# Optimization experiments

Hardware: AMD Instinct MI355X
Metric: run time of the kernel (lower is better)

## Reference

```python
import jax, jax.numpy as jnp
import numpy as np

B, T, D, H = 4, 2048, 512, 8
K = D // H  # head dim = 64

def setup_inputs() -> dict:
    key = jax.random.key(0)
    k1, k2, k3, k4 = jax.random.split(key, 4)
    x = jax.random.normal(k1, (B, T, D), dtype=jnp.float32)
    # torch nn.Linear stores weight as [out_features, in_features]
    w_qkv = jax.random.normal(k2, (3 * D, D), dtype=jnp.float32) * (D ** -0.5)
    w_proj = jax.random.normal(k3, (D, D), dtype=jnp.float32) * (D ** -0.5)
    b_proj = jax.random.normal(k4, (D,), dtype=jnp.float32) * 0.01
    return {"x": x, "w_qkv": w_qkv, "w_proj": w_proj, "b_proj": b_proj}

def reference(x, w_qkv, w_proj, b_proj):
    Bx, Tx, Dx = x.shape
    # qkv projection (no bias): [B,T,3D]
    qkv = jnp.einsum('btd,ed->bte', x, w_qkv)
    q, k, v = jnp.split(qkv, 3, axis=-1)
    # [B,H,T,K]
    def heads(t):
        return t.reshape(Bx, Tx, H, K).transpose(0, 2, 1, 3)
    q, k, v = heads(q), heads(k), heads(v)
    # scaled scores with causal mask
    scores = jnp.einsum('bhqk,bhsk->bhqs', q, k) * (K ** -0.5)  # [B,H,T,T]
    causal = jnp.tril(jnp.ones((Tx, Tx), dtype=bool))
    scores = jnp.where(causal, scores, -jnp.inf)
    attn = jax.nn.softmax(scores, axis=-1)  # dropout p=0.0 -> identity
    out = jnp.einsum('bhqs,bhsk->bhqk', attn, v)  # [B,H,T,K]
    out = out.transpose(0, 2, 1, 3).reshape(Bx, Tx, Dx)
    out = jnp.einsum('btd,ed->bte', out, w_proj) + b_proj
    return out
```

## Files before the change

kernel.cpp:

```cpp
#include <hip/hip_runtime.h>
#include <hip/hip_bf16.h>


typedef unsigned short u16;
typedef __attribute__((ext_vector_type(8))) __bf16 bf16x8;
typedef __attribute__((ext_vector_type(8))) unsigned short u16x8;
typedef __attribute__((ext_vector_type(4))) unsigned short u16x4;
typedef __attribute__((ext_vector_type(4))) float f32x4;
typedef __attribute__((ext_vector_type(4))) unsigned u32x4;
typedef __attribute__((ext_vector_type(2))) unsigned u32x2;

#define DEV static __device__ __forceinline__

DEV void async16(const u16* g, u16* l) {
  __builtin_amdgcn_global_load_lds(
      (const __attribute__((address_space(1))) unsigned int*)g,
      (__attribute__((address_space(3))) unsigned int*)l, 16, 0, 0);
}
DEV u16x8 gld8(const u16* p) { return *(const u16x8*)p; }
DEV void lst8(u16* p, u16x8 v) { *(u16x8*)p = v; }
DEV bf16x8 ldsld8(const u16* p) {
  return __builtin_bit_cast(bf16x8, *(const u16x8*)p);
}
DEV f32x4 mfma16(bf16x8 a, bf16x8 b, f32x4 c) {
  return __builtin_amdgcn_mfma_f32_16x16x32_bf16(a, b, c, 0, 0, 0);
}
DEV u16 f2b(float f) {
  unsigned u = __builtin_bit_cast(unsigned, f);
  u += 0x7FFFu + ((u >> 16) & 1u);
  return (u16)(u >> 16);
}
DEV unsigned pk2(float x, float y) {
  __hip_bfloat162 t = __float22bfloat162_rn(float2{x, y});
  unsigned r;
  __builtin_memcpy(&r, &t, 4);
  return r;
}
DEV u16x8 pack8(f32x4 a, f32x4 b) {
  u32x4 t;
  t[0] = pk2(a[0], a[1]);
  t[1] = pk2(a[2], a[3]);
  t[2] = pk2(b[0], b[1]);
  t[3] = pk2(b[2], b[3]);
  return __builtin_bit_cast(u16x8, t);
}
DEV void barrier_lgkm() {
  asm volatile("s_waitcnt lgkmcnt(0)" ::: "memory");
  __builtin_amdgcn_s_barrier();
  asm volatile("" ::: "memory");
}

__global__ void cvt_all(const float* __restrict__ x, const float* __restrict__ wq,
                        u16* __restrict__ xb, u16* __restrict__ wqb) {
  constexpr long NX = 8192L * 512 / 8;
  constexpr long NQ = 1536L * 512 / 8;
  const long i = (long)blockIdx.x * 256 + threadIdx.x;
  if (i < NX) {
    const float* p = x + i * 8;
    *(u16x8*)(xb + i * 8) = pack8(*(const f32x4*)p, *(const f32x4*)(p + 4));
  } else if (i < NX + NQ) {
    const long j = i - NX;
    const float* p = wq + j * 8;
    *(u16x8*)(wqb + j * 8) = pack8(*(const f32x4*)p, *(const f32x4*)(p + 4));
  }
}

__global__ void gemm_bb(const u16* __restrict__ A, const u16* __restrict__ Bt,
                        u16* __restrict__ qk, u16* __restrict__ vT, int K) {
  __shared__ __align__(16) u16 smem[17408];
  auto As = (u16(*)[128 * 32])smem;
  auto Bs = (u16(*)[128 * 32])(smem + 8192);
  u16* Cs = smem;
  constexpr int LDC = 136;

  const int t = threadIdx.x, lane = t & 63, w = t >> 6;
  const int lane15 = lane & 15, quad = lane >> 4;
  const int wr = w >> 1, wc = w & 1;

  const int i = blockIdx.x;
  const int rt = (i & 7) | (((i >> 3) & 7) << 3);
  const int ct = i >> 6;
  const long row0 = (long)rt * 128;
  const int col0 = ct * 128;

  const int srow = w * 16 + (lane >> 2);
  const int scol = (lane & 3) * 8;
  const u16* Ag = A + (row0 + srow) * (long)K + scol;
  const u16* Bg = Bt + ((long)col0 + srow) * (long)K + scol;

  f32x4 acc[4][4];
#pragma unroll
  for (int ii = 0; ii < 4; ii++)
#pragma unroll
    for (int j = 0; j < 4; j++) acc[ii][j] = (f32x4)(0.0f);

  for (int k0 = 0; k0 < K; k0 += 64) {
    __syncthreads();
#pragma unroll
    for (int r = 0; r < 2; r++)
#pragma unroll
      for (int hf = 0; hf < 2; hf++) {
        async16(Ag + (long)r * 64 * K + k0 + hf * 32,
                &As[hf][(r * 64 + w * 16) * 32]);
        async16(Bg + (long)r * 64 * K + k0 + hf * 32,
                &Bs[hf][(r * 64 + w * 16) * 32]);
      }
    __syncthreads();

#pragma unroll
    for (int hf = 0; hf < 2; hf++) {
      bf16x8 a[4], b[4];
#pragma unroll
      for (int ii = 0; ii < 4; ii++)
        a[ii] = ldsld8(&As[hf][(wr * 64 + ii * 16 + lane15) * 32 + quad * 8]);
#pragma unroll
      for (int j = 0; j < 4; j++)
        b[j] = ldsld8(&Bs[hf][(wc * 64 + j * 16 + lane15) * 32 + quad * 8]);
#pragma unroll
      for (int ii = 0; ii < 4; ii++)
#pragma unroll
        for (int j = 0; j < 4; j++) acc[ii][j] = mfma16(a[ii], b[j], acc[ii][j]);
    }
  }

  __syncthreads();

  if (col0 >= 1024) {
#pragma unroll
    for (int ii = 0; ii < 4; ii++)
#pragma unroll
      for (int j = 0; j < 4; j++) {
        const int d = wc * 64 + j * 16 + lane15;
        const int sl = wr * 64 + ii * 16 + quad * 4;
        const int psl =
            (sl & ~31) | (((sl >> 2) & 3) << 3) | (((sl >> 4) & 1) << 2);
        u32x2 pr;
        pr[0] = pk2(acc[ii][j][0], acc[ii][j][1]);
        pr[1] = pk2(acc[ii][j][2], acc[ii][j][3]);
        *(u16x4*)&Cs[d * LDC + psl] = __builtin_bit_cast(u16x4, pr);
      }
    __syncthreads();
    const long bb = row0 >> 11;
    const int s0g = (int)(row0 & 2047);
    const int rr = t >> 4, cc = (t & 15) * 8;
#pragma unroll
    for (int p = 0; p < 8; p++) {
      const int d = p * 16 + rr;
      *(u16x8*)(vT + ((bb * 512 + col0 - 1024 + d) * 2048L) + s0g + cc) =
          *(const u16x8*)&Cs[d * LDC + cc];
    }
  } else {
#pragma unroll
    for (int ii = 0; ii < 4; ii++)
#pragma unroll
      for (int j = 0; j < 4; j++) {
        const int c = wc * 64 + j * 16 + lane15;
        const float sc = (col0 + c < 512) ? 0.18033688f : 1.0f;
#pragma unroll
        for (int r = 0; r < 4; r++) {
          const int rw = wr * 64 + ii * 16 + quad * 4 + r;
          Cs[rw * LDC + c] = f2b(acc[ii][j][r] * sc);
        }
      }
    __syncthreads();
    const int rr = t >> 4, cc = (t & 15) * 8;
#pragma unroll
    for (int p = 0; p < 8; p++) {
      const int rw = p * 16 + rr;
      *(u16x8*)(qk + (row0 + rw) * 1024L + col0 + cc) =
          *(const u16x8*)&Cs[rw * LDC + cc];
    }
  }
}

__global__ void gemm_b64(const u16* __restrict__ A, const float* __restrict__ Bt,
                         const float* __restrict__ bias, float* __restrict__ C,
                         int N, int K) {
  __shared__ __align__(16) u16 smem[17408];
  auto As = (u16(*)[128 * 32])smem;
  auto Bs = (u16(*)[64 * 32])(smem + 8192);
  float* Cs = (float*)smem;
  constexpr int LDCF = 68;

  const int t = threadIdx.x, lane = t & 63, w = t >> 6;
  const int lane15 = lane & 15, quad = lane >> 4;
  const int wr = w >> 1, wc = w & 1;

  const int i = blockIdx.x;
  const int rt = (i & 7) | (((i >> 3) & 7) << 3);
  const int ct = i >> 6;
  const long row0 = (long)rt * 128;
  const int col0 = ct * 64;

  const int srow = w * 16 + (lane >> 2);
  const int scol = (lane & 3) * 8;
  const u16* Ag = A + (row0 + srow) * (long)K + scol;

  const int brow = t >> 2, bc = (t & 3) * 16;
  const float* Bg = Bt + (long)(col0 + brow) * K + bc;
  u16* BsD = &Bs[bc >> 5][brow * 32 + (bc & 31)];

  f32x4 acc[4][2];
#pragma unroll
  for (int ii = 0; ii < 4; ii++)
#pragma unroll
    for (int j = 0; j < 2; j++) acc[ii][j] = (f32x4)(0.0f);

  f32x4 q0 = *(const f32x4*)Bg, q1 = *(const f32x4*)(Bg + 4);
  f32x4 q2 = *(const f32x4*)(Bg + 8), q3 = *(const f32x4*)(Bg + 12);

  for (int k0 = 0; k0 < K; k0 += 64) {
    barrier_lgkm();
#pragma unroll
    for (int r = 0; r < 2; r++)
#pragma unroll
      for (int hf = 0; hf < 2; hf++)
        async16(Ag + (long)r * 64 * K + k0 + hf * 32,
                &As[hf][(r * 64 + w * 16) * 32]);
    lst8(BsD, pack8(q0, q1));
    lst8(BsD + 8, pack8(q2, q3));
    __syncthreads();

    {
      const int kp = (k0 + 64 < K) ? k0 + 64 : k0;
      q0 = *(const f32x4*)(Bg + kp);     q1 = *(const f32x4*)(Bg + kp + 4);
      q2 = *(const f32x4*)(Bg + kp + 8); q3 = *(const f32x4*)(Bg + kp + 12);
    }

#pragma unroll
    for (int hf = 0; hf < 2; hf++) {
      bf16x8 a[4], b[2];
#pragma unroll
      for (int ii = 0; ii < 4; ii++)
        a[ii] = ldsld8(&As[hf][(wr * 64 + ii * 16 + lane15) * 32 + quad * 8]);
#pragma unroll
      for (int j = 0; j < 2; j++)
        b[j] = ldsld8(&Bs[hf][(wc * 32 + j * 16 + lane15) * 32 + quad * 8]);
#pragma unroll
      for (int ii = 0; ii < 4; ii++)
#pragma unroll
        for (int j = 0; j < 2; j++) acc[ii][j] = mfma16(a[ii], b[j], acc[ii][j]);
    }
  }

  __syncthreads();
#pragma unroll
  for (int ii = 0; ii < 4; ii++)
#pragma unroll
    for (int j = 0; j < 2; j++) {
      const int c = wc * 32 + j * 16 + lane15;
      const float bv = bias[col0 + c];
#pragma unroll
      for (int r = 0; r < 4; r++) {
        const int rw = wr * 64 + ii * 16 + quad * 4 + r;
        Cs[rw * LDCF + c] = acc[ii][j][r] + bv;
      }
    }
  __syncthreads();
  const int rr = t >> 4, cc = (t & 15) * 4;
#pragma unroll
  for (int p = 0; p < 8; p++) {
    const int rw = p * 16 + rr;
    *(f32x4*)(C + (row0 + rw) * (long)N + col0 + cc) =
        *(const f32x4*)&Cs[rw * LDCF + cc];
  }
}

__global__ void __launch_bounds__(512, 4)
attn_v10(const u16* __restrict__ qk, const u16* __restrict__ vT,
         u16* __restrict__ out) {
  constexpr int T = 2048, LDQ = 1024;
  __shared__ __align__(16) u16 Ks[2][2][64 * 72];
  __shared__ __align__(16) u16 Vs[2][2][64 * 72];

  const int t = threadIdx.x, lane = t & 63, w = t >> 6;
  const int lane15 = lane & 15, quad = lane >> 4;
  const int half = w >> 2, wl = w & 3;

  const int i = blockIdx.x;
  int qb = i & 15;
  if (i >= 256) qb = 15 - qb;
  const int h = (i >> 4) & 7;
  const int b = (i >> 7) & 3;
  const long baseq = (long)b * T * LDQ;
  const u16* vTb = vT + ((long)b * 512 + h * 64) * 2048;

  const u16* gq =
      qk + baseq + (long)(qb * 128 + wl * 32 + lane15) * LDQ + h * 64 + quad * 8;
  const bf16x8 qa0 = __builtin_bit_cast(bf16x8, *(const u16x8*)gq);
  const bf16x8 qa1 = __builtin_bit_cast(bf16x8, *(const u16x8*)(gq + 32));
  const bf16x8 qc0 = __builtin_bit_cast(bf16x8, *(const u16x8*)(gq + 16 * LDQ));
  const bf16x8 qc1 =
      __builtin_bit_cast(bf16x8, *(const u16x8*)(gq + 16 * LDQ + 32));

  const int th = t & 255;
  const int srow = th >> 3, sc8 = (th & 7) * 8;
  const int nsbh = qb + 1;
  const int s0 = half * nsbh;
  const int sbd = 2 * qb + (wl >> 1);

  const u16* gk = qk + baseq + (long)(s0 * 64 + srow) * LDQ + 512 + h * 64 + sc8;
  const u16* gv = vTb + (long)srow * 2048 + s0 * 64 + sc8;

  u16x8 kr0, kr1, vr0, vr1;
  kr0 = gld8(gk); kr1 = gld8(gk + (long)32 * LDQ);
  vr0 = gld8(gv); vr1 = gld8(gv + (long)32 * 2048);
  lst8(&Ks[half][0][srow * 72 + sc8], kr0);
  lst8(&Ks[half][0][(srow + 32) * 72 + sc8], kr1);
  lst8(&Vs[half][0][srow * 72 + sc8], vr0);
  lst8(&Vs[half][0][(srow + 32) * 72 + sc8], vr1);
  if (nsbh > 1) { gk += (long)64 * LDQ; gv += 64; }
  kr0 = gld8(gk); kr1 = gld8(gk + (long)32 * LDQ);
  vr0 = gld8(gv); vr1 = gld8(gv + (long)32 * 2048);

  f32x4 o0[4], o1[4], lsum0 = (f32x4)(0.0f), lsum1 = (f32x4)(0.0f);
#pragma unroll
  for (int j = 0; j < 4; j++) { o0[j] = (f32x4)(0.0f); o1[j] = (f32x4)(0.0f); }

  const bf16x8 ones = __builtin_bit_cast(bf16x8, (u16x8)((u16)0x3F80));
  const int ql0 = ((wl & 1) << 5) + lane15;

  for (int it = 0; it < nsbh; ++it) {
    const u16* Kc = Ks[half][it & 1];
    const u16* Vc = Vs[half][it & 1];
    u16* Kn = Ks[half][(it + 1) & 1];
    u16* Vn = Vs[half][(it + 1) & 1];

    barrier_lgkm();

    lst8(&Kn[srow * 72 + sc8], kr0);
    lst8(&Kn[(srow + 32) * 72 + sc8], kr1);
    lst8(&Vn[srow * 72 + sc8], vr0);
    lst8(&Vn[(srow + 32) * 72 + sc8], vr1);

    if (it + 2 < nsbh) { gk += (long)64 * LDQ; gv += 64; }
    kr0 = gld8(gk); kr1 = gld8(gk + (long)32 * LDQ);
    vr0 = gld8(gv); vr1 = gld8(gv + (long)32 * 2048);

    const int sb = s0 + it;
    if (sb <= sbd) {
      __builtin_amdgcn_s_setprio(1);
      f32x4 sf0[4], sf1[4];
#pragma unroll
      for (int j = 0; j < 4; j++) {
        const bf16x8 k0 = ldsld8(&Kc[(j * 16 + lane15) * 72 + quad * 8]);
        const bf16x8 k1 = ldsld8(&Kc[(j * 16 + lane15) * 72 + quad * 8 + 32]);
        sf0[j] = mfma16(k1, qa1, mfma16(k0, qa0, (f32x4)(0.0f)));
        sf1[j] = mfma16(k1, qc1, mfma16(k0, qc0, (f32x4)(0.0f)));
      }

#pragma unroll
      for (int j = 0; j < 4; j++)
#pragma unroll
        for (int r = 0; r < 4; r++) {
          sf0[j][r] = exp2f(sf0[j][r]);
          sf1[j][r] = exp2f(sf1[j][r]);
        }
      if (sb == sbd) {
#pragma unroll
        for (int j = 0; j < 4; j++)
#pragma unroll
          for (int r = 0; r < 4; r++) {
            const int sl = j * 16 + quad * 4 + r;
            if (sl > ql0) sf0[j][r] = 0.0f;
            if (sl > ql0 + 16) sf1[j][r] = 0.0f;
          }
      }

      u32x4 w0, w1, w2, w3;
      w0[0] = pk2(sf0[0][0], sf0[0][1]); w0[1] = pk2(sf0[0][2], sf0[0][3]);
      w0[2] = pk2(sf0[1][0], sf0[1][1]); w0[3] = pk2(sf0[1][2], sf0[1][3]);
      w1[0] = pk2(sf0[2][0], sf0[2][1]); w1[1] = pk2(sf0[2][2], sf0[2][3]);
      w1[2] = pk2(sf0[3][0], sf0[3][1]); w1[3] = pk2(sf0[3][2], sf0[3][3]);
      w2[0] = pk2(sf1[0][0], sf1[0][1]); w2[1] = pk2(sf1[0][2], sf1[0][3]);
      w2[2] = pk2(sf1[1][0], sf1[1][1]); w2[3] = pk2(sf1[1][2], sf1[1][3]);
      w3[0] = pk2(sf1[2][0], sf1[2][1]); w3[1] = pk2(sf1[2][2], sf1[2][3]);
      w3[2] = pk2(sf1[3][0], sf1[3][1]); w3[3] = pk2(sf1[3][2], sf1[3][3]);
      const bf16x8 pa0 = __builtin_bit_cast(bf16x8, w0);
      const bf16x8 pa1 = __builtin_bit_cast(bf16x8, w1);
      const bf16x8 pc0 = __builtin_bit_cast(bf16x8, w2);
      const bf16x8 pc1 = __builtin_bit_cast(bf16x8, w3);

#pragma unroll
      for (int j = 0; j < 4; j++) {
        const int d0 = (j * 16 + lane15) * 72;
        const bf16x8 v0 = ldsld8(&Vc[d0 + quad * 8]);
        const bf16x8 v1 = ldsld8(&Vc[d0 + quad * 8 + 32]);
        o0[j] = mfma16(pa1, v1, mfma16(pa0, v0, o0[j]));
        o1[j] = mfma16(pc1, v1, mfma16(pc0, v0, o1[j]));
      }
      lsum0 = mfma16(pa1, ones, mfma16(pa0, ones, lsum0));
      lsum1 = mfma16(pc1, ones, mfma16(pc0, ones, lsum1));
      __builtin_amdgcn_s_setprio(0);
    }
  }

  barrier_lgkm();
  float* cmb = (float*)&Ks[0][0][0];
  float* cl = (float*)&Vs[0][0][0];

  if (half == 1) {
    const int q0 = wl * 32 + quad * 4;
#pragma unroll
    for (int j = 0; j < 4; j++)
#pragma unroll
      for (int r = 0; r < 4; r++) {
        cmb[(q0 + r) * 64 + j * 16 + lane15] = o0[j][r];
        cmb[(q0 + 16 + r) * 64 + j * 16 + lane15] = o1[j][r];
      }
    if (lane15 == 0) {
#pragma unroll
      for (int r = 0; r < 4; r++) {
        cl[q0 + r] = lsum0[r];
        cl[q0 + 16 + r] = lsum1[r];
      }
    }
  }
  barrier_lgkm();

  if (half == 0) {
    const int q0 = wl * 32 + quad * 4;
    f32x4 inv0, inv1;
#pragma unroll
    for (int r = 0; r < 4; r++) {
      inv0[r] = 1.0f / (lsum0[r] + cl[q0 + r]);
      inv1[r] = 1.0f / (lsum1[r] + cl[q0 + 16 + r]);
    }
    const long orow0 = (long)b * T + qb * 128 + wl * 32;
#pragma unroll
    for (int j = 0; j < 4; j++)
#pragma unroll
      for (int r = 0; r < 4; r++) {
        const float a0 = o0[j][r] + cmb[(q0 + r) * 64 + j * 16 + lane15];
        const float a1 = o1[j][r] + cmb[(q0 + 16 + r) * 64 + j * 16 + lane15];
        const long rr = orow0 + quad * 4 + r;
        out[rr * 512 + h * 64 + j * 16 + lane15] = f2b(a0 * inv0[r]);
        out[(rr + 16) * 512 + h * 64 + j * 16 + lane15] = f2b(a1 * inv1[r]);
      }
  }
}

extern "C" void kernel_launch(void* const* d_in, const int* in_sizes, int n_in,
                              void* d_out, int out_size, void* d_ws, size_t ws_size,
                              hipStream_t stream) {
  const float* x      = (const float*)d_in[0];
  const float* w_qkv  = (const float*)d_in[1];
  const float* w_proj = (const float*)d_in[2];
  const float* b_proj = (const float*)d_in[3];
  float* out = (float*)d_out;

  u16* qk = (u16*)d_ws;
  u16* vT = qk + (size_t)8192 * 1024;
  u16* xb = vT + (size_t)4 * 512 * 2048;
  u16* wqb = (u16*)d_out;

  cvt_all<<<2432, 256, 0, stream>>>(x, w_qkv, xb, wqb);
  gemm_bb<<<768, 256, 0, stream>>>(xb, wqb, qk, vT, 512);
  attn_v10<<<512, 512, 0, stream>>>(qk, vT, xb);
  gemm_b64<<<512, 256, 0, stream>>>(xb, w_proj, b_proj, out, 512, 512);
}
```

Before: 142.8 us.

## Load K/V tiles with async global-to-LDS copies and an XOR-swizzled layout

The attention kernel now copies K and V tiles straight from global memory into LDS with global_load_lds, replacing the old path that loaded into registers and then stored to LDS. The padded 72-element row stride is replaced by an unpadded 64-element stride with an XOR swizzle of 16-byte chunks, and the reads are remapped to match. The goal is to drop the register staging and the separate LDS store instructions while avoiding bank conflicts with a smaller LDS footprint. In exchange, the prefetch now only overlaps with one iteration of compute, because the next __syncthreads waits for the async loads. The smaller K/V buffers are also reused as scratch for the final combine, which could be too small.

```diff
diff --git a/kernel.cpp b/kernel.cpp
--- a/kernel.cpp
+++ b/kernel.cpp
@@ -267,11 +267,11 @@
 }
 
 __global__ void __launch_bounds__(512, 4)
-attn_v10(const u16* __restrict__ qk, const u16* __restrict__ vT,
+attn_v11(const u16* __restrict__ qk, const u16* __restrict__ vT,
          u16* __restrict__ out) {
   constexpr int T = 2048, LDQ = 1024;
-  __shared__ __align__(16) u16 Ks[2][2][64 * 72];
-  __shared__ __align__(16) u16 Vs[2][2][64 * 72];
+  __shared__ __align__(16) u16 Ks[2][2][64 * 64];
+  __shared__ __align__(16) u16 Vs[2][2][64 * 64];
 
   const int t = threadIdx.x, lane = t & 63, w = t >> 6;
   const int lane15 = lane & 15, quad = lane >> 4;
@@ -294,24 +294,24 @@
       __builtin_bit_cast(bf16x8, *(const u16x8*)(gq + 16 * LDQ + 32));
 
   const int th = t & 255;
-  const int srow = th >> 3, sc8 = (th & 7) * 8;
+  const int srow = th >> 3;
+  const int scs = (th & 7) ^ (srow & 7);
   const int nsbh = qb + 1;
   const int s0 = half * nsbh;
   const int sbd = 2 * qb + (wl >> 1);
 
-  const u16* gk = qk + baseq + (long)(s0 * 64 + srow) * LDQ + 512 + h * 64 + sc8;
-  const u16* gv = vTb + (long)srow * 2048 + s0 * 64 + sc8;
-
-  u16x8 kr0, kr1, vr0, vr1;
-  kr0 = gld8(gk); kr1 = gld8(gk + (long)32 * LDQ);
-  vr0 = gld8(gv); vr1 = gld8(gv + (long)32 * 2048);
-  lst8(&Ks[half][0][srow * 72 + sc8], kr0);
-  lst8(&Ks[half][0][(srow + 32) * 72 + sc8], kr1);
-  lst8(&Vs[half][0][srow * 72 + sc8], vr0);
-  lst8(&Vs[half][0][(srow + 32) * 72 + sc8], vr1);
-  if (nsbh > 1) { gk += (long)64 * LDQ; gv += 64; }
-  kr0 = gld8(gk); kr1 = gld8(gk + (long)32 * LDQ);
-  vr0 = gld8(gv); vr1 = gld8(gv + (long)32 * 2048);
+  const u16* ksrc = qk + baseq + (long)(s0 * 64 + srow) * LDQ + 512 + h * 64 + scs * 8;
+  const u16* vsrc = vTb + (long)srow * 2048 + s0 * 64 + scs * 8;
+  const int ldst = th * 8;
+
+  {
+    u16* kd = &Ks[half][0][0];
+    u16* vd = &Vs[half][0][0];
+    async16(ksrc, kd + ldst);
+    async16(ksrc + (long)32 * LDQ, kd + 2048 + ldst);
+    async16(vsrc, vd + ldst);
+    async16(vsrc + (long)32 * 2048, vd + 2048 + ldst);
+  }
 
   f32x4 o0[4], o1[4], lsum0 = (f32x4)(0.0f), lsum1 = (f32x4)(0.0f);
 #pragma unroll
@@ -319,32 +319,33 @@
 
   const bf16x8 ones = __builtin_bit_cast(bf16x8, (u16x8)((u16)0x3F80));
   const int ql0 = ((wl & 1) << 5) + lane15;
+  const int cs = (quad ^ (lane15 & 7)) * 8;
 
   for (int it = 0; it < nsbh; ++it) {
-    const u16* Kc = Ks[half][it & 1];
-    const u16* Vc = Vs[half][it & 1];
-    u16* Kn = Ks[half][(it + 1) & 1];
-    u16* Vn = Vs[half][(it + 1) & 1];
-
-    barrier_lgkm();
-
-    lst8(&Kn[srow * 72 + sc8], kr0);
-    lst8(&Kn[(srow + 32) * 72 + sc8], kr1);
-    lst8(&Vn[srow * 72 + sc8], vr0);
-    lst8(&Vn[(srow + 32) * 72 + sc8], vr1);
-
-    if (it + 2 < nsbh) { gk += (long)64 * LDQ; gv += 64; }
-    kr0 = gld8(gk); kr1 = gld8(gk + (long)32 * LDQ);
-    vr0 = gld8(gv); vr1 = gld8(gv + (long)32 * 2048);
+    __syncthreads();
+
+    if (it + 1 < nsbh) {
+      ksrc += (long)64 * LDQ;
+      vsrc += 64;
+      u16* kd = &Ks[half][(it + 1) & 1][0];
+      u16* vd = &Vs[half][(it + 1) & 1][0];
+      async16(ksrc, kd + ldst);
+      async16(ksrc + (long)32 * LDQ, kd + 2048 + ldst);
+      async16(vsrc, vd + ldst);
+      async16(vsrc + (long)32 * 2048, vd + 2048 + ldst);
+    }
 
     const int sb = s0 + it;
     if (sb <= sbd) {
+      const u16* Kc = Ks[half][it & 1];
+      const u16* Vc = Vs[half][it & 1];
       __builtin_amdgcn_s_setprio(1);
       f32x4 sf0[4], sf1[4];
 #pragma unroll
       for (int j = 0; j < 4; j++) {
-        const bf16x8 k0 = ldsld8(&Kc[(j * 16 + lane15) * 72 + quad * 8]);
-        const bf16x8 k1 = ldsld8(&Kc[(j * 16 + lane15) * 72 + quad * 8 + 32]);
+        const int rb = (j * 16 + lane15) * 64;
+        const bf16x8 k0 = ldsld8(&Kc[rb + cs]);
+        const bf16x8 k1 = ldsld8(&Kc[rb + (cs ^ 32)]);
         sf0[j] = mfma16(k1, qa1, mfma16(k0, qa0, (f32x4)(0.0f)));
         sf1[j] = mfma16(k1, qc1, mfma16(k0, qc0, (f32x4)(0.0f)));
       }
@@ -383,9 +384,9 @@
 
 #pragma unroll
       for (int j = 0; j < 4; j++) {
-        const int d0 = (j * 16 + lane15) * 72;
-        const bf16x8 v0 = ldsld8(&Vc[d0 + quad * 8]);
-        const bf16x8 v1 = ldsld8(&Vc[d0 + quad * 8 + 32]);
+        const int rb = (j * 16 + lane15) * 64;
+        const bf16x8 v0 = ldsld8(&Vc[rb + cs]);
+        const bf16x8 v1 = ldsld8(&Vc[rb + (cs ^ 32)]);
         o0[j] = mfma16(pa1, v1, mfma16(pa0, v0, o0[j]));
         o1[j] = mfma16(pc1, v1, mfma16(pc0, v0, o1[j]));
       }
@@ -456,6 +457,6 @@
 
   cvt_all<<<2432, 256, 0, stream>>>(x, w_qkv, xb, wqb);
   gemm_bb<<<768, 256, 0, stream>>>(xb, wqb, qk, vT, 512);
-  attn_v10<<<512, 512, 0, stream>>>(qk, vT, xb);
+  attn_v11<<<512, 512, 0, stream>>>(qk, vT, xb);
   gemm_b64<<<512, 256, 0, stream>>>(xb, w_proj, b_proj, out, 512, 512);
 }
```

Measured after the change: 146.6 us. +2.7%, slower.

## Load K/V fragments directly from global memory instead of LDS double-buffering

Applied to the files above, without the earlier changes.

The attention kernel no longer stages K and V tiles through double-buffered shared memory with per-iteration barriers. Each wave now loads its K and V MFMA fragments straight from global memory (relying on L2 and L1 for reuse) and trims the loop to the blocks it actually needs, removing the barrier and the skipped-iteration overhead. Shared memory is kept only for the final cross-half combine. In exchange, global and L2 traffic goes up because the four waves in a half each reload the same K/V data, and load latency is no longer hidden by prefetch. There is also a risk that the combine step loses the barrier it needs, since barrier_lgkm was removed before it.

```diff
diff --git a/kernel.cpp b/kernel.cpp
--- a/kernel.cpp
+++ b/kernel.cpp
@@ -20,6 +20,9 @@
 DEV u16x8 gld8(const u16* p) { return *(const u16x8*)p; }
 DEV void lst8(u16* p, u16x8 v) { *(u16x8*)p = v; }
 DEV bf16x8 ldsld8(const u16* p) {
+  return __builtin_bit_cast(bf16x8, *(const u16x8*)p);
+}
+DEV bf16x8 gldb8(const u16* p) {
   return __builtin_bit_cast(bf16x8, *(const u16x8*)p);
 }
 DEV f32x4 mfma16(bf16x8 a, bf16x8 b, f32x4 c) {
@@ -267,11 +270,11 @@
 }
 
 __global__ void __launch_bounds__(512, 4)
-attn_v10(const u16* __restrict__ qk, const u16* __restrict__ vT,
+attn_v12(const u16* __restrict__ qk, const u16* __restrict__ vT,
          u16* __restrict__ out) {
   constexpr int T = 2048, LDQ = 1024;
-  __shared__ __align__(16) u16 Ks[2][2][64 * 72];
-  __shared__ __align__(16) u16 Vs[2][2][64 * 72];
+  __shared__ __align__(16) float cmb[128 * 64];
+  __shared__ float cl[128];
 
   const int t = threadIdx.x, lane = t & 63, w = t >> 6;
   const int lane15 = lane & 15, quad = lane >> 4;
@@ -287,31 +290,20 @@
 
   const u16* gq =
       qk + baseq + (long)(qb * 128 + wl * 32 + lane15) * LDQ + h * 64 + quad * 8;
-  const bf16x8 qa0 = __builtin_bit_cast(bf16x8, *(const u16x8*)gq);
-  const bf16x8 qa1 = __builtin_bit_cast(bf16x8, *(const u16x8*)(gq + 32));
-  const bf16x8 qc0 = __builtin_bit_cast(bf16x8, *(const u16x8*)(gq + 16 * LDQ));
-  const bf16x8 qc1 =
-      __builtin_bit_cast(bf16x8, *(const u16x8*)(gq + 16 * LDQ + 32));
-
-  const int th = t & 255;
-  const int srow = th >> 3, sc8 = (th & 7) * 8;
+  const bf16x8 qa0 = gldb8(gq);
+  const bf16x8 qa1 = gldb8(gq + 32);
+  const bf16x8 qc0 = gldb8(gq + 16 * LDQ);
+  const bf16x8 qc1 = gldb8(gq + 16 * LDQ + 32);
+
   const int nsbh = qb + 1;
   const int s0 = half * nsbh;
   const int sbd = 2 * qb + (wl >> 1);
-
-  const u16* gk = qk + baseq + (long)(s0 * 64 + srow) * LDQ + 512 + h * 64 + sc8;
-  const u16* gv = vTb + (long)srow * 2048 + s0 * 64 + sc8;
-
-  u16x8 kr0, kr1, vr0, vr1;
-  kr0 = gld8(gk); kr1 = gld8(gk + (long)32 * LDQ);
-  vr0 = gld8(gv); vr1 = gld8(gv + (long)32 * 2048);
-  lst8(&Ks[half][0][srow * 72 + sc8], kr0);
-  lst8(&Ks[half][0][(srow + 32) * 72 + sc8], kr1);
-  lst8(&Vs[half][0][srow * 72 + sc8], vr0);
-  lst8(&Vs[half][0][(srow + 32) * 72 + sc8], vr1);
-  if (nsbh > 1) { gk += (long)64 * LDQ; gv += 64; }
-  kr0 = gld8(gk); kr1 = gld8(gk + (long)32 * LDQ);
-  vr0 = gld8(gv); vr1 = gld8(gv + (long)32 * 2048);
+  int nit = sbd - s0 + 1;
+  if (nit > nsbh) nit = nsbh;
+
+  const u16* kb =
+      qk + baseq + (long)(s0 * 64 + lane15) * LDQ + 512 + h * 64 + quad * 8;
+  const u16* vb = vTb + (long)lane15 * 2048 + s0 * 64 + quad * 8;
 
   f32x4 o0[4], o1[4], lsum0 = (f32x4)(0.0f), lsum1 = (f32x4)(0.0f);
 #pragma unroll
@@ -320,84 +312,75 @@
   const bf16x8 ones = __builtin_bit_cast(bf16x8, (u16x8)((u16)0x3F80));
   const int ql0 = ((wl & 1) << 5) + lane15;
 
-  for (int it = 0; it < nsbh; ++it) {
-    const u16* Kc = Ks[half][it & 1];
-    const u16* Vc = Vs[half][it & 1];
-    u16* Kn = Ks[half][(it + 1) & 1];
-    u16* Vn = Vs[half][(it + 1) & 1];
-
-    barrier_lgkm();
-
-    lst8(&Kn[srow * 72 + sc8], kr0);
-    lst8(&Kn[(srow + 32) * 72 + sc8], kr1);
-    lst8(&Vn[srow * 72 + sc8], vr0);
-    lst8(&Vn[(srow + 32) * 72 + sc8], vr1);
-
-    if (it + 2 < nsbh) { gk += (long)64 * LDQ; gv += 64; }
-    kr0 = gld8(gk); kr1 = gld8(gk + (long)32 * LDQ);
-    vr0 = gld8(gv); vr1 = gld8(gv + (long)32 * 2048);
-
+  for (int it = 0; it < nit; ++it) {
     const int sb = s0 + it;
-    if (sb <= sbd) {
-      __builtin_amdgcn_s_setprio(1);
-      f32x4 sf0[4], sf1[4];
-#pragma unroll
-      for (int j = 0; j < 4; j++) {
-        const bf16x8 k0 = ldsld8(&Kc[(j * 16 + lane15) * 72 + quad * 8]);
-        const bf16x8 k1 = ldsld8(&Kc[(j * 16 + lane15) * 72 + quad * 8 + 32]);
-        sf0[j] = mfma16(k1, qa1, mfma16(k0, qa0, (f32x4)(0.0f)));
-        sf1[j] = mfma16(k1, qc1, mfma16(k0, qc0, (f32x4)(0.0f)));
-      }
-
+    __builtin_amdgcn_s_setprio(1);
+
+    bf16x8 k0[4], k1[4];
+#pragma unroll
+    for (int j = 0; j < 4; j++) {
+      k0[j] = gldb8(kb + (long)(j * 16) * LDQ);
+      k1[j] = gldb8(kb + (long)(j * 16) * LDQ + 32);
+    }
+    kb += (long)64 * LDQ;
+
+    f32x4 sf0[4], sf1[4];
+#pragma unroll
+    for (int j = 0; j < 4; j++)
+      sf0[j] = mfma16(k1[j], qa1, mfma16(k0[j], qa0, (f32x4)(0.0f)));
+#pragma unroll
+    for (int j = 0; j < 4; j++)
+      sf1[j] = mfma16(k1[j], qc1, mfma16(k0[j], qc0, (f32x4)(0.0f)));
+
+#pragma unroll
+    for (int j = 0; j < 4; j++)
+#pragma unroll
+      for (int r = 0; r < 4; r++) {
+        sf0[j][r] = exp2f(sf0[j][r]);
+        sf1[j][r] = exp2f(sf1[j][r]);
+      }
+    if (sb == sbd) {
 #pragma unroll
       for (int j = 0; j < 4; j++)
 #pragma unroll
         for (int r = 0; r < 4; r++) {
-          sf0[j][r] = exp2f(sf0[j][r]);
-          sf1[j][r] = exp2f(sf1[j][r]);
+          const int sl = j * 16 + quad * 4 + r;
+          if (sl > ql0) sf0[j][r] = 0.0f;
+          if (sl > ql0 + 16) sf1[j][r] = 0.0f;
         }
-      if (sb == sbd) {
-#pragma unroll
-        for (int j = 0; j < 4; j++)
-#pragma unroll
-          for (int r = 0; r < 4; r++) {
-            const int sl = j * 16 + quad * 4 + r;
-            if (sl > ql0) sf0[j][r] = 0.0f;
-            if (sl > ql0 + 16) sf1[j][r] = 0.0f;
-          }
-      }
-
-      u32x4 w0, w1, w2, w3;
-      w0[0] = pk2(sf0[0][0], sf0[0][1]); w0[1] = pk2(sf0[0][2], sf0[0][3]);
-      w0[2] = pk2(sf0[1][0], sf0[1][1]); w0[3] = pk2(sf0[1][2], sf0[1][3]);
-      w1[0] = pk2(sf0[2][0], sf0[2][1]); w1[1] = pk2(sf0[2][2], sf0[2][3]);
-      w1[2] = pk2(sf0[3][0], sf0[3][1]); w1[3] = pk2(sf0[3][2], sf0[3][3]);
-      w2[0] = pk2(sf1[0][0], sf1[0][1]); w2[1] = pk2(sf1[0][2], sf1[0][3]);
-      w2[2] = pk2(sf1[1][0], sf1[1][1]); w2[3] = pk2(sf1[1][2], sf1[1][3]);
-      w3[0] = pk2(sf1[2][0], sf1[2][1]); w3[1] = pk2(sf1[2][2], sf1[2][3]);
-      w3[2] = pk2(sf1[3][0], sf1[3][1]); w3[3] = pk2(sf1[3][2], sf1[3][3]);
-      const bf16x8 pa0 = __builtin_bit_cast(bf16x8, w0);
-      const bf16x8 pa1 = __builtin_bit_cast(bf16x8, w1);
-      const bf16x8 pc0 = __builtin_bit_cast(bf16x8, w2);
-      const bf16x8 pc1 = __builtin_bit_cast(bf16x8, w3);
-
-#pragma unroll
-      for (int j = 0; j < 4; j++) {
-        const int d0 = (j * 16 + lane15) * 72;
-        const bf16x8 v0 = ldsld8(&Vc[d0 + quad * 8]);
-        const bf16x8 v1 = ldsld8(&Vc[d0 + quad * 8 + 32]);
-        o0[j] = mfma16(pa1, v1, mfma16(pa0, v0, o0[j]));
-        o1[j] = mfma16(pc1, v1, mfma16(pc0, v0, o1[j]));
-      }
-      lsum0 = mfma16(pa1, ones, mfma16(pa0, ones, lsum0));
-      lsum1 = mfma16(pc1, ones, mfma16(pc0, ones, lsum1));
-      __builtin_amdgcn_s_setprio(0);
-    }
-  }
-
-  barrier_lgkm();
-  float* cmb = (float*)&Ks[0][0][0];
-  float* cl = (float*)&Vs[0][0][0];
+    }
+
+    u32x4 w0, w1, w2, w3;
+    w0[0] = pk2(sf0[0][0], sf0[0][1]); w0[1] = pk2(sf0[0][2], sf0[0][3]);
+    w0[2] = pk2(sf0[1][0], sf0[1][1]); w0[3] = pk2(sf0[1][2], sf0[1][3]);
+    w1[0] = pk2(sf0[2][0], sf0[2][1]); w1[1] = pk2(sf0[2][2], sf0[2][3]);
+    w1[2] = pk2(sf0[3][0], sf0[3][1]); w1[3] = pk2(sf0[3][2], sf0[3][3]);
+    w2[0] = pk2(sf1[0][0], sf1[0][1]); w2[1] = pk2(sf1[0][2], sf1[0][3]);
+    w2[2] = pk2(sf1[1][0], sf1[1][1]); w2[3] = pk2(sf1[1][2], sf1[1][3]);
+    w3[0] = pk2(sf1[2][0], sf1[2][1]); w3[1] = pk2(sf1[2][2], sf1[2][3]);
+    w3[2] = pk2(sf1[3][0], sf1[3][1]); w3[3] = pk2(sf1[3][2], sf1[3][3]);
+    const bf16x8 pa0 = __builtin_bit_cast(bf16x8, w0);
+    const bf16x8 pa1 = __builtin_bit_cast(bf16x8, w1);
+    const bf16x8 pc0 = __builtin_bit_cast(bf16x8, w2);
+    const bf16x8 pc1 = __builtin_bit_cast(bf16x8, w3);
+
+    bf16x8 v0[4], v1[4];
+#pragma unroll
+    for (int j = 0; j < 4; j++) {
+      v0[j] = gldb8(vb + (long)(j * 16) * 2048);
+      v1[j] = gldb8(vb + (long)(j * 16) * 2048 + 32);
+    }
+    vb += 64;
+
+#pragma unroll
+    for (int j = 0; j < 4; j++) {
+      o0[j] = mfma16(pa1, v1[j], mfma16(pa0, v0[j], o0[j]));
+      o1[j] = mfma16(pc1, v1[j], mfma16(pc0, v0[j], o1[j]));
+    }
+    lsum0 = mfma16(pa1, ones, mfma16(pa0, ones, lsum0));
+    lsum1 = mfma16(pc1, ones, mfma16(pc0, ones, lsum1));
+    __builtin_amdgcn_s_setprio(0);
+  }
 
   if (half == 1) {
     const int q0 = wl * 32 + quad * 4;
@@ -456,6 +439,6 @@
 
   cvt_all<<<2432, 256, 0, stream>>>(x, w_qkv, xb, wqb);
   gemm_bb<<<768, 256, 0, stream>>>(xb, wqb, qk, vT, 512);
-  attn_v10<<<512, 512, 0, stream>>>(qk, vT, xb);
+  attn_v12<<<512, 512, 0, stream>>>(qk, vT, xb);
   gemm_b64<<<512, 256, 0, stream>>>(xb, w_proj, b_proj, out, 512, 512);
 }
```

After: 171.8 us. 1.2x slower.
